# Optimization experiments

Hardware: AMD Instinct MI355X
Metric: run time of the kernel (lower is better)

The kernel has to match this reference:

```python
import jax, jax.numpy as jnp
import numpy as np

SHAPES = ((96, 144), (48, 72), (24, 36), (12, 18))
BS, EMBED = 2, 256
HEADS, LEVELS, POINTS = 8, 4, 4
NEMBED = EMBED // HEADS
LEN_V = sum(h * w for h, w in SHAPES)
LEN_Q = LEN_V  # encoder self-attention: every pixel is a query


def _pos_grid_init():
    # Faithful re-implementation of MultiScaleDeformableAttention.pos_grid_init
    thetas = jnp.arange(HEADS, dtype=jnp.float32) * (2.0 * np.pi / HEADS)
    g = jnp.stack([jnp.cos(thetas), jnp.sin(thetas)], -1)
    g = g / jnp.max(jnp.abs(g), axis=-1, keepdims=True)
    g = jnp.tile(g.reshape(HEADS, 1, 1, 2), (1, LEVELS, POINTS, 1))
    scale = (jnp.arange(POINTS, dtype=jnp.float32) + 1.0)[None, None, :, None]
    return g * scale  # [HEADS, LEVELS, POINTS, 2]


def setup_inputs() -> dict:
    ks = jax.random.split(jax.random.key(0), 7)
    return {
        'query': jax.random.normal(ks[0], (BS, LEN_Q, EMBED), jnp.float32),
        'ref_points': jax.random.uniform(ks[1], (BS, LEN_Q, LEVELS, 2), jnp.float32),
        'value': jax.random.normal(ks[2], (BS, LEN_V, EMBED), jnp.float32),
        'pad_mask': jnp.ones((BS, LEN_V), dtype=bool),
        'value_proj_kernel': jax.random.normal(ks[3], (EMBED, HEADS, NEMBED), jnp.float32) * 0.05,
        'value_proj_bias': jnp.zeros((HEADS, NEMBED), jnp.float32),
        'sampling_offsets_kernel': jax.random.normal(ks[4], (EMBED, HEADS, LEVELS, POINTS, 2), jnp.float32) * 0.01,
        'sampling_offsets_bias': _pos_grid_init(),
        'attn_kernel': jax.random.normal(ks[5], (EMBED, HEADS, LEVELS * POINTS), jnp.float32) * 0.02,
        'attn_bias': jnp.zeros((HEADS, LEVELS * POINTS), jnp.float32),
        'out_kernel': jax.random.normal(ks[6], (HEADS, NEMBED, EMBED), jnp.float32) * 0.05,
        'out_bias': jnp.zeros((EMBED,), jnp.float32),
        'train': 0,
    }


def _bilinear(im, grid, w, h):
    """Batched 2D bilinear interpolation, zero outside the image.

    im:   [B, h*w, e] flattened feature map
    grid: [B, N, 2] normalized coords (pixel centers at (x+0.5)/w, (y+0.5)/h)
    Returns [B, N, e]. Identical math to the original gather-based kernel:
    out-of-bounds corner weights are zeroed, so zero-padding the image by 1
    reproduces the 'empty'-pad + masked-weight scheme exactly.
    """
    B, _, e = im.shape
    imp = jnp.pad(im.reshape(B, h, w, e), ((0, 0), (1, 1), (1, 1), (0, 0)))
    imp = imp.reshape(B, (h + 2) * (w + 2), e)
    x = grid[..., 0] * w - 0.5
    y = grid[..., 1] * h - 0.5
    x0 = jnp.floor(x).astype(jnp.int32)
    y0 = jnp.floor(y).astype(jnp.int32)
    x1 = x0 + 1
    y1 = y0 + 1

    def gather(yy, xx):
        idx = jnp.clip(yy + 1, 0, h + 1) * (w + 2) + jnp.clip(xx + 1, 0, w + 1)
        return jnp.take_along_axis(imp, idx[..., None], axis=1)  # [B, N, e]

    x0f, y0f = x0.astype(x.dtype), y0.astype(y.dtype)
    x1f, y1f = x1.astype(x.dtype), y1.astype(y.dtype)
    inx0 = (x0 >= 0) & (x0 <= w - 1)
    inx1 = (x1 >= 0) & (x1 <= w - 1)
    iny0 = (y0 >= 0) & (y0 <= h - 1)
    iny1 = (y1 >= 0) & (y1 <= h - 1)
    wa = jnp.where(inx0 & iny0, (x1f - x) * (y1f - y), 0.0)
    wb = jnp.where(inx0 & iny1, (x1f - x) * (y - y0f), 0.0)
    wc = jnp.where(inx1 & iny0, (x - x0f) * (y1f - y), 0.0)
    wd = jnp.where(inx1 & iny1, (x - x0f) * (y - y0f), 0.0)
    return (gather(y0, x0) * wa[..., None] + gather(y1, x0) * wb[..., None]
            + gather(y0, x1) * wc[..., None] + gather(y1, x1) * wd[..., None])


def _forward(query, ref_points, value, pad_mask, vpk, vpb, sok, sob, ak, ab, okern, obias):
    bs, len_q, _ = query.shape
    len_v = value.shape[1]
    # value projection + pad masking -> [bs*H, len_v, nembed]
    v = jnp.einsum('bve,ehd->bvhd', value, vpk) + vpb
    v = jnp.where(pad_mask[..., None, None], v, 0)
    v = v.transpose(0, 2, 1, 3).reshape(bs * HEADS, len_v, NEMBED)
    # sampling locations (ref_dim == 2 branch) -> [bs*H, L, P*len_q, 2]
    off = jnp.einsum('bqe,ehlpc->bqhlpc', query, sok) + sob
    offset_norm = jnp.array([[w, h] for h, w in SHAPES], dtype=query.dtype)  # [L, 2]
    loc = ref_points[:, :, None, :, None, :] + off / offset_norm[None, None, None, :, None, :]
    loc = loc.transpose(0, 2, 3, 4, 1, 5).reshape(bs * HEADS, LEVELS, POINTS * len_q, 2)
    # attention weights (softmax over L*P) -> [bs*H, len_q, L*P]
    aw = jnp.einsum('bqe,ehm->bqhm', query, ak) + ab
    aw = jax.nn.softmax(aw, axis=-1)
    aw = aw.transpose(0, 2, 1, 3).reshape(bs * HEADS, len_q, LEVELS * POINTS)
    # per-level bilinear sampling, concatenated level-major over (level, point)
    starts = np.cumsum([0] + [h * w for h, w in SHAPES])
    sampled = []
    for li, (h, w) in enumerate(SHAPES):
        vl = v[:, starts[li]:starts[li + 1], :]
        s = _bilinear(vl, loc[:, li], w, h)  # [bs*H, P*len_q, nembed]
        sampled.append(s.reshape(bs * HEADS, POINTS, len_q, NEMBED))
    sampled = jnp.concatenate(sampled, axis=1)  # [bs*H, L*P, len_q, nembed]
    x = jnp.einsum('blqe,bql->bqe', sampled, aw)
    x = x.reshape(bs, HEADS, len_q, NEMBED)
    # output projection: DenseGeneral over (heads, nembed)
    return jnp.einsum('bhqe,hed->bqd', x, okern) + obias


def reference(query, ref_points, value, pad_mask, value_proj_kernel, value_proj_bias,
              sampling_offsets_kernel, sampling_offsets_bias, attn_kernel, attn_bias,
              out_kernel, out_bias, train):
    del train  # eval mode (no remat); math is identical
    return _forward(query, ref_points, value, pad_mask, value_proj_kernel, value_proj_bias,
                    sampling_offsets_kernel, sampling_offsets_bias, attn_kernel, attn_bias,
                    out_kernel, out_bias)
```

## Files before the change

kernel.cpp:

```cpp
#include <hip/hip_runtime.h>
#include <math.h>

#define LEN 18360
#define M_ROWS (2 * LEN)
#define NTASK (16 * LEN)

typedef unsigned short u16;
typedef __attribute__((ext_vector_type(8))) short bf16x8;
typedef __attribute__((ext_vector_type(4))) float f32x4;

__device__ __forceinline__ u16 f2bf(float f) {
  unsigned u = __float_as_uint(f);
  return (u16)((u + 0x7fffu + ((u >> 16) & 1u)) >> 16);
}
__device__ __forceinline__ u16 f2h(float f) {
  union { _Float16 h; u16 u; } c;
  c.h = (_Float16)f;
  return c.u;
}
__device__ __forceinline__ void async_cp16(const void* g, void* l) {
  __builtin_amdgcn_global_load_lds(
      (const __attribute__((address_space(1))) unsigned*)g,
      (__attribute__((address_space(3))) unsigned*)l, 16, 0, 0);
}

#define MIX_LO(acc, word, wf)                                           \
  asm("v_fma_mix_f32 %0, %1, %2, %0 op_sel:[0,0,0] op_sel_hi:[1,0,0]"  \
      : "+v"(acc)                                                       \
      : "v"(word), "v"(wf))
#define MIX_HI(acc, word, wf)                                           \
  asm("v_fma_mix_f32 %0, %1, %2, %0 op_sel:[1,0,0] op_sel_hi:[1,0,0]"  \
      : "+v"(acc)                                                       \
      : "v"(word), "v"(wf))

__global__ __launch_bounds__(256) void gemm_mfma_k(
    const u16* __restrict__ A0, const u16* __restrict__ Bt0,
    const float* __restrict__ bias0, void* __restrict__ C0, int N0, int nt0,
    int mode0, int split, const u16* __restrict__ A1,
    const u16* __restrict__ Bt1, const float* __restrict__ bias1,
    void* __restrict__ C1, int N1, int nt1, int mode1) {
  __shared__ u16 A_lds[2][8 * 512];
  __shared__ u16 B_lds[2][8 * 512];

  int bid = (int)blockIdx.x;
  const u16* A;
  const u16* Bt;
  const float* bias;
  void* Cv;
  int N, nt, mode;
  if (bid < split) {
    A = A0; Bt = Bt0; bias = bias0; Cv = C0; N = N0; nt = nt0; mode = mode0;
  } else {
    bid -= split;
    A = A1; Bt = Bt1; bias = bias1; Cv = C1; N = N1; nt = nt1; mode = mode1;
  }
  const int n0 = (bid % nt) << 7;
  const int m0 = (bid / nt) << 7;

  const int tid = threadIdx.x;
  const int w = tid >> 6;
  const int lane = tid & 63;
  const int wm = w & 1, wn = w >> 1;
  const int mr = lane & 15;
  const int kq = (lane >> 4) * 8;

  const int st0 = 2 * w;
  const int ga0 = min(m0 + st0 * 16 + mr, M_ROWS - 1);
  const int ga1 = min(m0 + (st0 + 1) * 16 + mr, M_ROWS - 1);
  const int gb0 = n0 + st0 * 16 + mr;
  const int gb1 = n0 + (st0 + 1) * 16 + mr;
  const u16* pa0 = A + (size_t)ga0 * 256 + kq;
  const u16* pa1 = A + (size_t)ga1 * 256 + kq;
  const u16* pb0 = Bt + (size_t)gb0 * 256 + kq;
  const u16* pb1 = Bt + (size_t)gb1 * 256 + kq;

  f32x4 acc[4][4];
#pragma unroll
  for (int i = 0; i < 4; i++)
#pragma unroll
    for (int j = 0; j < 4; j++) acc[i][j] = (f32x4){0.f, 0.f, 0.f, 0.f};

  async_cp16(pa0, &A_lds[0][st0 * 512]);
  async_cp16(pa1, &A_lds[0][(st0 + 1) * 512]);
  async_cp16(pb0, &B_lds[0][st0 * 512]);
  async_cp16(pb1, &B_lds[0][(st0 + 1) * 512]);
  __syncthreads();

#pragma unroll
  for (int kt = 0; kt < 8; kt++) {
    const int cur = kt & 1;
    if (kt < 7) {
      const int k0 = (kt + 1) << 5;
      async_cp16(pa0 + k0, &A_lds[cur ^ 1][st0 * 512]);
      async_cp16(pa1 + k0, &A_lds[cur ^ 1][(st0 + 1) * 512]);
      async_cp16(pb0 + k0, &B_lds[cur ^ 1][st0 * 512]);
      async_cp16(pb1 + k0, &B_lds[cur ^ 1][(st0 + 1) * 512]);
    }
    bf16x8 af[4], bf[4];
#pragma unroll
    for (int i = 0; i < 4; i++)
      af[i] = *(const bf16x8*)&A_lds[cur][(wm * 4 + i) * 512 + lane * 8];
#pragma unroll
    for (int j = 0; j < 4; j++)
      bf[j] = *(const bf16x8*)&B_lds[cur][(wn * 4 + j) * 512 + lane * 8];
#pragma unroll
    for (int i = 0; i < 4; i++)
#pragma unroll
      for (int j = 0; j < 4; j++)
        acc[i][j] = __builtin_amdgcn_mfma_f32_16x16x32_bf16(bf[j], af[i],
                                                            acc[i][j], 0, 0, 0);
    if (kt < 7) __syncthreads();
  }

#pragma unroll
  for (int i = 0; i < 4; i++) {
    const int row = m0 + wm * 64 + i * 16 + mr;
    if (row >= M_ROWS) continue;
#pragma unroll
    for (int j = 0; j < 4; j++) {
      const int col = n0 + wn * 64 + j * 16 + (lane >> 4) * 4;
      const float4 b4 = *(const float4*)(bias + col);
      float4 o;
      o.x = acc[i][j][0] + b4.x;
      o.y = acc[i][j][1] + b4.y;
      o.z = acc[i][j][2] + b4.z;
      o.w = acc[i][j][3] + b4.w;
      if (mode == 0) {
        *(float4*)((float*)Cv + (size_t)row * N + col) = o;
      } else if (mode == 1) {
        const int b = row >= LEN;
        const int lv = row - b * LEN;
        const int h = col >> 5, d = col & 31;
        uint2 p;
        p.x = (unsigned)f2h(o.x) | ((unsigned)f2h(o.y) << 16);
        p.y = (unsigned)f2h(o.z) | ((unsigned)f2h(o.w) << 16);
        *(uint2*)((u16*)Cv + ((size_t)((b * 8 + h) * LEN + lv)) * 32 + d) = p;
      } else {
        uint2 p;
        p.x = (unsigned)f2bf(o.x) | ((unsigned)f2bf(o.y) << 16);
        p.y = (unsigned)f2bf(o.z) | ((unsigned)f2bf(o.w) << 16);
        *(uint2*)((u16*)Cv + (size_t)row * N + col) = p;
      }
    }
  }
}

__global__ __launch_bounds__(256) void cast_qv_k(const float* __restrict__ q,
                                                 const float* __restrict__ v,
                                                 u16* __restrict__ qb,
                                                 u16* __restrict__ vb) {
  const size_t i = ((size_t)blockIdx.x * 256 + threadIdx.x) * 4;
  float4 a = *(const float4*)(q + i);
  uint2 p;
  p.x = (unsigned)f2bf(a.x) | ((unsigned)f2bf(a.y) << 16);
  p.y = (unsigned)f2bf(a.z) | ((unsigned)f2bf(a.w) << 16);
  *(uint2*)&qb[i] = p;
  float4 c = *(const float4*)(v + i);
  p.x = (unsigned)f2bf(c.x) | ((unsigned)f2bf(c.y) << 16);
  p.y = (unsigned)f2bf(c.z) | ((unsigned)f2bf(c.w) << 16);
  *(uint2*)&vb[i] = p;
}

__global__ __launch_bounds__(256) void wcast_k(
    const float* __restrict__ vpk, const float* __restrict__ sok,
    const float* __restrict__ ak, const float* __restrict__ ok,
    const float* __restrict__ sob, const float* __restrict__ ab,
    u16* __restrict__ vpk_t, u16* __restrict__ sa_t, u16* __restrict__ ok_t,
    float* __restrict__ bias_cat) {
  const int gid = blockIdx.x * 256 + threadIdx.x;
  if (gid < 65536) {
    const int d = gid, n = d >> 8, k = d & 255;
    vpk_t[d] = f2bf(vpk[k * 256 + n]);
  } else if (gid < 131072) {
    const int d = gid - 65536, n = d >> 8, k = d & 255;
    sa_t[d] = f2bf(sok[k * 256 + n]);
  } else if (gid < 163840) {
    const int d = gid - 131072, n = d >> 8, k = d & 255;
    sa_t[65536 + d] = f2bf(ak[k * 128 + n]);
  } else if (gid < 229376) {
    const int d = gid - 163840, n = d >> 8, k = d & 255;
    ok_t[d] = f2bf(ok[k * 256 + n]);
  } else if (gid < 229760) {
    const int d = gid - 229376;
    bias_cat[d] = (d < 256) ? sob[d] : ab[d - 256];
  }
}

__global__ __launch_bounds__(256) void sampler_k(
    const u16* __restrict__ v,
    const u16* __restrict__ offaw,
    const float* __restrict__ refp,
    u16* __restrict__ xb)
{
  __shared__ int2 meta[4 * 544];
  const int tid = threadIdx.x;
  const int wv = tid >> 6;
  const int lane = tid & 63;
  int2* const mw = &meta[wv * 544];

  const int bid0 = (int)blockIdx.x;
  const int xcd = bid0 & 7;
  const int within = bid0 >> 3;
  const int bid =
      (xcd < 4 ? xcd * 1148 : 4 * 1148 + (xcd - 4) * 1147) + within;

#pragma unroll
  for (int rep = 0; rep < 2; rep++) {
    const int t4 = lane >> 4;
    const int s = lane & 15;
    const int l = s >> 2;
    const int tl = (rep << 2) + t4;

    const int task = (bid << 5) + (wv << 3) + tl;
    const int q = task % LEN;
// ... 78 lines not shown
      mA2 = mrowA[s + 1];
      mB2 = mrowB[s + 1];
      pA2 = *(const uint4*)(vb + (unsigned)mA2.x + dqo);
      pB2 = *(const uint4*)(vb + (unsigned)mB2.x + dqo);
    }
    const float wA = __int_as_float(mA.y);
    const float wB = __int_as_float(mB.y);
    MIX_LO(a0, pA.x, wA);
    MIX_HI(a1, pA.x, wA);
    MIX_LO(a2, pA.y, wA);
    MIX_HI(a3, pA.y, wA);
    MIX_LO(a4, pA.z, wA);
    MIX_HI(a5, pA.z, wA);
    MIX_LO(a6, pA.w, wA);
    MIX_HI(a7, pA.w, wA);
    MIX_LO(a0, pB.x, wB);
    MIX_HI(a1, pB.x, wB);
    MIX_LO(a2, pB.y, wB);
    MIX_HI(a3, pB.y, wB);
    MIX_LO(a4, pB.z, wB);
    MIX_HI(a5, pB.z, wB);
    MIX_LO(a6, pB.w, wB);
    MIX_HI(a7, pB.w, wB);
    mA = mA2; mB = mB2; pA = pA2; pB = pB2;
  }

  a0 += __shfl_xor(a0, 4); a1 += __shfl_xor(a1, 4);
  a2 += __shfl_xor(a2, 4); a3 += __shfl_xor(a3, 4);
  a4 += __shfl_xor(a4, 4); a5 += __shfl_xor(a5, 4);
  a6 += __shfl_xor(a6, 4); a7 += __shfl_xor(a7, 4);

  if (c2 == 0) {
    uint4 o;
    o.x = (unsigned)f2bf(a0) | ((unsigned)f2bf(a1) << 16);
    o.y = (unsigned)f2bf(a2) | ((unsigned)f2bf(a3) << 16);
    o.z = (unsigned)f2bf(a4) | ((unsigned)f2bf(a5) << 16);
    o.w = (unsigned)f2bf(a6) | ((unsigned)f2bf(a7) << 16);
    *(uint4*)&xb[qrow * 256 + h * 32 + (dq << 3)] = o;
  }
}

extern "C" void kernel_launch(void* const* d_in, const int* in_sizes, int n_in,
                              void* d_out, int out_size, void* d_ws,
                              size_t ws_size, hipStream_t stream) {
  (void)in_sizes; (void)n_in; (void)out_size; (void)ws_size;

  const float* query = (const float*)d_in[0];
  const float* refp = (const float*)d_in[1];
  const float* value = (const float*)d_in[2];
  const float* vpk = (const float*)d_in[4];
  const float* vpb = (const float*)d_in[5];
  const float* sok = (const float*)d_in[6];
  const float* sob = (const float*)d_in[7];
  const float* ak = (const float*)d_in[8];
  const float* ab = (const float*)d_in[9];
  const float* okern = (const float*)d_in[10];
  const float* obias = (const float*)d_in[11];

  char* p = (char*)d_ws;
  u16* v_ws = (u16*)p;   p += (size_t)M_ROWS * 256 * 2;
  u16* offaw = (u16*)p;  p += (size_t)M_ROWS * 384 * 2;
  u16* qbf = (u16*)p;    p += (size_t)M_ROWS * 256 * 2;
  u16* vbf = (u16*)p;    p += (size_t)M_ROWS * 256 * 2;
  u16* vpk_t = (u16*)p;  p += 65536 * 2;
  u16* sa_t = (u16*)p;   p += 98304 * 2;
  u16* ok_t = (u16*)p;   p += 65536 * 2;
  float* bias_cat = (float*)p;
  u16* x_b = qbf;

  const dim3 blk(256);
  const int mt = (M_ROWS + 127) / 128;

  cast_qv_k<<<dim3(2350080 / 256), blk, 0, stream>>>(query, value, qbf, vbf);
  wcast_k<<<dim3(898), blk, 0, stream>>>(vpk, sok, ak, okern, sob, ab, vpk_t,
                                         sa_t, ok_t, bias_cat);
  gemm_mfma_k<<<dim3(2 * mt + 3 * mt), blk, 0, stream>>>(
      vbf, vpk_t, vpb, v_ws, 256, 2, 1, 2 * mt,
      qbf, sa_t, bias_cat, offaw, 384, 3, 2);
  sampler_k<<<dim3(NTASK / 32), blk, 0, stream>>>(v_ws, offaw, refp, x_b);
  gemm_mfma_k<<<dim3(2 * mt), blk, 0, stream>>>(
      x_b, ok_t, obias, (float*)d_out, 256, 2, 0, 2 * mt,
      x_b, ok_t, obias, (float*)d_out, 256, 2, 0);
}
```

Baseline: 254.2 us.

## Fuse fp32-to-bf16 input cast into GEMM A-tile loads and remap blocks per XCD

Removes the separate cast kernel for query and value. The projection GEMM now reads fp32 A rows directly, converts them to bf16 in registers, and writes them to LDS, with the next tile's loads issued before the MFMAs. This saves one launch and a full write and re-read of the bf16 copies. Block IDs are also remapped so that consecutive tiles land on the same XCD, to improve L2 locality. In exchange, the fp32 A loads go through registers instead of async LDS copies, which raises VGPR pressure and adds conversion ALU work inside the GEMM.

Result: no change. 251.7 us (-1.0%).

```diff
diff --git a/kernel.cpp b/kernel.cpp
--- a/kernel.cpp
+++ b/kernel.cpp
@@ -33,26 +33,35 @@
       : "+v"(acc)                                                       \
       : "v"(word), "v"(wf))
 
+__device__ __forceinline__ int xcd_chunk_remap(int bid0, int nwg) {
+  const int q = nwg >> 3, r = nwg & 7;
+  const int xcd = bid0 & 7;
+  const int wi = bid0 >> 3;
+  return (xcd < r ? xcd * (q + 1) : r * (q + 1) + (xcd - r) * q) + wi;
+}
+
 __global__ __launch_bounds__(256) void gemm_mfma_k(
-    const u16* __restrict__ A0, const u16* __restrict__ Bt0,
+    const void* __restrict__ A0, const u16* __restrict__ Bt0,
     const float* __restrict__ bias0, void* __restrict__ C0, int N0, int nt0,
-    int mode0, int split, const u16* __restrict__ A1,
+    int mode0, int af0, int split, const void* __restrict__ A1,
     const u16* __restrict__ Bt1, const float* __restrict__ bias1,
-    void* __restrict__ C1, int N1, int nt1, int mode1) {
+    void* __restrict__ C1, int N1, int nt1, int mode1, int af1) {
   __shared__ u16 A_lds[2][8 * 512];
   __shared__ u16 B_lds[2][8 * 512];
 
-  int bid = (int)blockIdx.x;
-  const u16* A;
+  int bid = xcd_chunk_remap((int)blockIdx.x, (int)gridDim.x);
+  const void* Av;
   const u16* Bt;
   const float* bias;
   void* Cv;
-  int N, nt, mode;
+  int N, nt, mode, af;
   if (bid < split) {
-    A = A0; Bt = Bt0; bias = bias0; Cv = C0; N = N0; nt = nt0; mode = mode0;
+    Av = A0; Bt = Bt0; bias = bias0; Cv = C0; N = N0; nt = nt0; mode = mode0;
+    af = af0;
   } else {
     bid -= split;
-    A = A1; Bt = Bt1; bias = bias1; Cv = C1; N = N1; nt = nt1; mode = mode1;
+    Av = A1; Bt = Bt1; bias = bias1; Cv = C1; N = N1; nt = nt1; mode = mode1;
+    af = af1;
   }
   const int n0 = (bid % nt) << 7;
   const int m0 = (bid / nt) << 7;
@@ -69,10 +78,16 @@
   const int ga1 = min(m0 + (st0 + 1) * 16 + mr, M_ROWS - 1);
   const int gb0 = n0 + st0 * 16 + mr;
   const int gb1 = n0 + (st0 + 1) * 16 + mr;
-  const u16* pa0 = A + (size_t)ga0 * 256 + kq;
-  const u16* pa1 = A + (size_t)ga1 * 256 + kq;
+  const u16* ba0 = (const u16*)Av + (size_t)ga0 * 256 + kq;
+  const u16* ba1 = (const u16*)Av + (size_t)ga1 * 256 + kq;
+  const float* fa0 = (const float*)Av + (size_t)ga0 * 256 + kq;
+  const float* fa1 = (const float*)Av + (size_t)ga1 * 256 + kq;
   const u16* pb0 = Bt + (size_t)gb0 * 256 + kq;
   const u16* pb1 = Bt + (size_t)gb1 * 256 + kq;
+  u16* const la0 = &A_lds[0][st0 * 512 + lane * 8];
+  u16* const la1 = &A_lds[0][(st0 + 1) * 512 + lane * 8];
+  u16* const lb0 = &A_lds[1][st0 * 512 + lane * 8];
+  u16* const lb1 = &A_lds[1][(st0 + 1) * 512 + lane * 8];
 
   f32x4 acc[4][4];
 #pragma unroll
@@ -80,8 +95,26 @@
 #pragma unroll
     for (int j = 0; j < 4; j++) acc[i][j] = (f32x4){0.f, 0.f, 0.f, 0.f};
 
-  async_cp16(pa0, &A_lds[0][st0 * 512]);
-  async_cp16(pa1, &A_lds[0][(st0 + 1) * 512]);
+  if (af) {
+    const float4 f0 = *(const float4*)(fa0);
+    const float4 f1 = *(const float4*)(fa0 + 4);
+    const float4 g0 = *(const float4*)(fa1);
+    const float4 g1 = *(const float4*)(fa1 + 4);
+    uint4 pk;
+    pk.x = (unsigned)f2bf(f0.x) | ((unsigned)f2bf(f0.y) << 16);
+    pk.y = (unsigned)f2bf(f0.z) | ((unsigned)f2bf(f0.w) << 16);
+    pk.z = (unsigned)f2bf(f1.x) | ((unsigned)f2bf(f1.y) << 16);
+    pk.w = (unsigned)f2bf(f1.z) | ((unsigned)f2bf(f1.w) << 16);
+    *(uint4*)la0 = pk;
+    pk.x = (unsigned)f2bf(g0.x) | ((unsigned)f2bf(g0.y) << 16);
+    pk.y = (unsigned)f2bf(g0.z) | ((unsigned)f2bf(g0.w) << 16);
+    pk.z = (unsigned)f2bf(g1.x) | ((unsigned)f2bf(g1.y) << 16);
+    pk.w = (unsigned)f2bf(g1.z) | ((unsigned)f2bf(g1.w) << 16);
+    *(uint4*)la1 = pk;
+  } else {
+    async_cp16(ba0, &A_lds[0][st0 * 512]);
+    async_cp16(ba1, &A_lds[0][(st0 + 1) * 512]);
+  }
   async_cp16(pb0, &B_lds[0][st0 * 512]);
   async_cp16(pb1, &B_lds[0][(st0 + 1) * 512]);
   __syncthreads();
@@ -89,26 +122,47 @@
 #pragma unroll
   for (int kt = 0; kt < 8; kt++) {
     const int cur = kt & 1;
+    const int kn = (kt + 1) << 5;
+    float4 f0, f1, g0, g1;
     if (kt < 7) {
-      const int k0 = (kt + 1) << 5;
-      async_cp16(pa0 + k0, &A_lds[cur ^ 1][st0 * 512]);
-      async_cp16(pa1 + k0, &A_lds[cur ^ 1][(st0 + 1) * 512]);
-      async_cp16(pb0 + k0, &B_lds[cur ^ 1][st0 * 512]);
-      async_cp16(pb1 + k0, &B_lds[cur ^ 1][(st0 + 1) * 512]);
+      if (af) {
+        f0 = *(const float4*)(fa0 + kn);
+        f1 = *(const float4*)(fa0 + kn + 4);
+        g0 = *(const float4*)(fa1 + kn);
+        g1 = *(const float4*)(fa1 + kn + 4);
+      } else {
+        async_cp16(ba0 + kn, &A_lds[cur ^ 1][st0 * 512]);
+        async_cp16(ba1 + kn, &A_lds[cur ^ 1][(st0 + 1) * 512]);
+      }
+      async_cp16(pb0 + kn, &B_lds[cur ^ 1][st0 * 512]);
+      async_cp16(pb1 + kn, &B_lds[cur ^ 1][(st0 + 1) * 512]);
     }
-    bf16x8 af[4], bf[4];
+    bf16x8 afr[4], bfr[4];
 #pragma unroll
     for (int i = 0; i < 4; i++)
-      af[i] = *(const bf16x8*)&A_lds[cur][(wm * 4 + i) * 512 + lane * 8];
+      afr[i] = *(const bf16x8*)&A_lds[cur][(wm * 4 + i) * 512 + lane * 8];
 #pragma unroll
     for (int j = 0; j < 4; j++)
-      bf[j] = *(const bf16x8*)&B_lds[cur][(wn * 4 + j) * 512 + lane * 8];
+      bfr[j] = *(const bf16x8*)&B_lds[cur][(wn * 4 + j) * 512 + lane * 8];
 #pragma unroll
     for (int i = 0; i < 4; i++)
 #pragma unroll
       for (int j = 0; j < 4; j++)
-        acc[i][j] = __builtin_amdgcn_mfma_f32_16x16x32_bf16(bf[j], af[i],
+        acc[i][j] = __builtin_amdgcn_mfma_f32_16x16x32_bf16(bfr[j], afr[i],
                                                             acc[i][j], 0, 0, 0);
+    if (kt < 7 && af) {
+      uint4 pk;
+      pk.x = (unsigned)f2bf(f0.x) | ((unsigned)f2bf(f0.y) << 16);
+      pk.y = (unsigned)f2bf(f0.z) | ((unsigned)f2bf(f0.w) << 16);
+      pk.z = (unsigned)f2bf(f1.x) | ((unsigned)f2bf(f1.y) << 16);
+      pk.w = (unsigned)f2bf(f1.z) | ((unsigned)f2bf(f1.w) << 16);
+      *(uint4*)(cur ? la0 : lb0) = pk;
+      pk.x = (unsigned)f2bf(g0.x) | ((unsigned)f2bf(g0.y) << 16);
+      pk.y = (unsigned)f2bf(g0.z) | ((unsigned)f2bf(g0.w) << 16);
+      pk.z = (unsigned)f2bf(g1.x) | ((unsigned)f2bf(g1.y) << 16);
+      pk.w = (unsigned)f2bf(g1.z) | ((unsigned)f2bf(g1.w) << 16);
+      *(uint4*)(cur ? la1 : lb1) = pk;
+    }
     if (kt < 7) __syncthreads();
   }
 
@@ -143,22 +197,6 @@
       }
     }
   }
-}
-
-__global__ __launch_bounds__(256) void cast_qv_k(const float* __restrict__ q,
-                                                 const float* __restrict__ v,
-                                                 u16* __restrict__ qb,
-                                                 u16* __restrict__ vb) {
-  const size_t i = ((size_t)blockIdx.x * 256 + threadIdx.x) * 4;
-  float4 a = *(const float4*)(q + i);
-  uint2 p;
-  p.x = (unsigned)f2bf(a.x) | ((unsigned)f2bf(a.y) << 16);
-  p.y = (unsigned)f2bf(a.z) | ((unsigned)f2bf(a.w) << 16);
-  *(uint2*)&qb[i] = p;
-  float4 c = *(const float4*)(v + i);
-  p.x = (unsigned)f2bf(c.x) | ((unsigned)f2bf(c.y) << 16);
-  p.y = (unsigned)f2bf(c.z) | ((unsigned)f2bf(c.w) << 16);
-  *(uint2*)&vb[i] = p;
 }
 
 __global__ __launch_bounds__(256) void wcast_k(
@@ -352,25 +390,22 @@
   char* p = (char*)d_ws;
   u16* v_ws = (u16*)p;   p += (size_t)M_ROWS * 256 * 2;
   u16* offaw = (u16*)p;  p += (size_t)M_ROWS * 384 * 2;
-  u16* qbf = (u16*)p;    p += (size_t)M_ROWS * 256 * 2;
-  u16* vbf = (u16*)p;    p += (size_t)M_ROWS * 256 * 2;
+  u16* x_ws = (u16*)p;   p += (size_t)M_ROWS * 256 * 2;
   u16* vpk_t = (u16*)p;  p += 65536 * 2;
   u16* sa_t = (u16*)p;   p += 98304 * 2;
   u16* ok_t = (u16*)p;   p += 65536 * 2;
   float* bias_cat = (float*)p;
-  u16* x_b = qbf;
 
   const dim3 blk(256);
   const int mt = (M_ROWS + 127) / 128;
 
-  cast_qv_k<<<dim3(2350080 / 256), blk, 0, stream>>>(query, value, qbf, vbf);
   wcast_k<<<dim3(898), blk, 0, stream>>>(vpk, sok, ak, okern, sob, ab, vpk_t,
                                          sa_t, ok_t, bias_cat);
   gemm_mfma_k<<<dim3(2 * mt + 3 * mt), blk, 0, stream>>>(
-      vbf, vpk_t, vpb, v_ws, 256, 2, 1, 2 * mt,
-      qbf, sa_t, bias_cat, offaw, 384, 3, 2);
-  sampler_k<<<dim3(NTASK / 32), blk, 0, stream>>>(v_ws, offaw, refp, x_b);
+      value, vpk_t, vpb, v_ws, 256, 2, 1, 1, 2 * mt,
+      query, sa_t, bias_cat, offaw, 384, 3, 2, 1);
+  sampler_k<<<dim3(NTASK / 32), blk, 0, stream>>>(v_ws, offaw, refp, x_ws);
   gemm_mfma_k<<<dim3(2 * mt), blk, 0, stream>>>(
-      x_b, ok_t, obias, (float*)d_out, 256, 2, 0, 2 * mt,
-      x_b, ok_t, obias, (float*)d_out, 256, 2, 0);
-}
+      x_ws, ok_t, obias, (float*)d_out, 256, 2, 0, 0, 2 * mt,
+      x_ws, ok_t, obias, (float*)d_out, 256, 2, 0, 0);
+}
```

## Fuse fp32-to-bf16 cast into persistent GEMM with resident B tiles

Applied to the files above, without the earlier changes.

Removes the separate query/value cast kernel. The first GEMM now loads fp32 activations directly and packs them to bf16 in registers before writing LDS. Both GEMMs become persistent kernels that keep the full 128-column B slice in LDS, loop over several M tiles with register double-buffered A loads, and remap block IDs so that chunks stay on one XCD. This trades a larger LDS footprint (about 80KB per block, lowering occupancy) and fp32 A traffic inside the GEMM for dropping one launch, the bf16 intermediate writes and reads, and repeated B loads.

After: 284.7 us. 12.0% more time.

```diff
diff --git a/kernel.cpp b/kernel.cpp
--- a/kernel.cpp
+++ b/kernel.cpp
@@ -4,14 +4,15 @@
 #define LEN 18360
 #define M_ROWS (2 * LEN)
 #define NTASK (16 * LEN)
+#define MT_TOT 287
 
 typedef unsigned short u16;
 typedef __attribute__((ext_vector_type(8))) short bf16x8;
 typedef __attribute__((ext_vector_type(4))) float f32x4;
 
-__device__ __forceinline__ u16 f2bf(float f) {
+__device__ __forceinline__ unsigned f2bf(float f) {
   unsigned u = __float_as_uint(f);
-  return (u16)((u + 0x7fffu + ((u >> 16) & 1u)) >> 16);
+  return (u + 0x7fffu + ((u >> 16) & 1u)) >> 16;
 }
 __device__ __forceinline__ u16 f2h(float f) {
   union { _Float16 h; u16 u; } c;
@@ -33,29 +34,42 @@
       : "+v"(acc)                                                       \
       : "v"(word), "v"(wf))
 
-__global__ __launch_bounds__(256) void gemm_mfma_k(
-    const u16* __restrict__ A0, const u16* __restrict__ Bt0,
-    const float* __restrict__ bias0, void* __restrict__ C0, int N0, int nt0,
-    int mode0, int split, const u16* __restrict__ A1,
-    const u16* __restrict__ Bt1, const float* __restrict__ bias1,
-    void* __restrict__ C1, int N1, int nt1, int mode1) {
-  __shared__ u16 A_lds[2][8 * 512];
-  __shared__ u16 B_lds[2][8 * 512];
-
-  int bid = (int)blockIdx.x;
-  const u16* A;
+__device__ __forceinline__ int xcd_chunk_remap(int bid0, int nwg) {
+  const int q = nwg >> 3, r = nwg & 7;
+  const int xcd = bid0 & 7;
+  const int wi = bid0 >> 3;
+  return (xcd < r ? xcd * (q + 1) : r * (q + 1) + (xcd - r) * q) + wi;
+}
+
+template <int AF>
+__global__ __launch_bounds__(256) void gemm_persist_k(
+    const void* __restrict__ A0, const u16* __restrict__ Bt0,
+    const float* __restrict__ bias0, void* __restrict__ C0, int N0, int mode0,
+    int lanes0, const void* __restrict__ A1, const u16* __restrict__ Bt1,
+    const float* __restrict__ bias1, void* __restrict__ C1, int N1, int mode1,
+    int NL, int J) {
+  __shared__ u16 B_all[8 * 4096];
+  __shared__ u16 A_lds[2][4096];
+
+  const int r = xcd_chunk_remap((int)blockIdx.x, (int)gridDim.x);
+  const int j = r / NL;
+  const int lane_n = r % NL;
+
+  const void* Av;
   const u16* Bt;
   const float* bias;
   void* Cv;
-  int N, nt, mode;
-  if (bid < split) {
-    A = A0; Bt = Bt0; bias = bias0; Cv = C0; N = N0; nt = nt0; mode = mode0;
+  int N, mode, ncol;
+  if (lane_n < lanes0) {
+    Av = A0; Bt = Bt0; bias = bias0; Cv = C0; N = N0; mode = mode0;
+    ncol = lane_n;
   } else {
-    bid -= split;
-    A = A1; Bt = Bt1; bias = bias1; Cv = C1; N = N1; nt = nt1; mode = mode1;
-  }
-  const int n0 = (bid % nt) << 7;
-  const int m0 = (bid / nt) << 7;
+    Av = A1; Bt = Bt1; bias = bias1; Cv = C1; N = N1; mode = mode1;
+    ncol = lane_n - lanes0;
+  }
+  const int n0 = ncol << 7;
+  const int nmt = (MT_TOT - j + J - 1) / J;
+  const int total = nmt << 3;
 
   const int tid = threadIdx.x;
   const int w = tid >> 6;
@@ -63,102 +77,143 @@
   const int wm = w & 1, wn = w >> 1;
   const int mr = lane & 15;
   const int kq = (lane >> 4) * 8;
-
   const int st0 = 2 * w;
-  const int ga0 = min(m0 + st0 * 16 + mr, M_ROWS - 1);
-  const int ga1 = min(m0 + (st0 + 1) * 16 + mr, M_ROWS - 1);
-  const int gb0 = n0 + st0 * 16 + mr;
-  const int gb1 = n0 + (st0 + 1) * 16 + mr;
-  const u16* pa0 = A + (size_t)ga0 * 256 + kq;
-  const u16* pa1 = A + (size_t)ga1 * 256 + kq;
-  const u16* pb0 = Bt + (size_t)gb0 * 256 + kq;
-  const u16* pb1 = Bt + (size_t)gb1 * 256 + kq;
+
+#pragma unroll
+  for (int kt = 0; kt < 8; kt++) {
+#pragma unroll
+    for (int t = 0; t < 2; t++) {
+      const int st = st0 + t;
+      const int gb = n0 + st * 16 + mr;
+      async_cp16(Bt + (size_t)gb * 256 + kt * 32 + kq,
+                 &B_all[kt * 4096 + st * 512]);
+    }
+  }
+
+  float4 Ef0, Ef1, Eg0, Eg1, Of0, Of1, Og0, Og1;
+  uint4 Ea, Eb, Oa, Ob;
+
+#define LOAD_STEP(u, q0, q1, q2, q3, b0, b1)                          \
+  {                                                                   \
+    const int m0c = (j + ((u) >> 3) * J) << 7;                        \
+    const int ga0c = min(m0c + st0 * 16 + mr, M_ROWS - 1);            \
+    const int ga1c = min(m0c + (st0 + 1) * 16 + mr, M_ROWS - 1);      \
+    const int ko = ((u) & 7) * 32 + kq;                               \
+    if (AF) {                                                         \
+      const float* fA0 = (const float*)Av + (size_t)ga0c * 256 + ko;  \
+      const float* fA1 = (const float*)Av + (size_t)ga1c * 256 + ko;  \
+      q0 = *(const float4*)fA0;                                       \
+      q1 = *(const float4*)(fA0 + 4);                                 \
+      q2 = *(const float4*)fA1;                                       \
+      q3 = *(const float4*)(fA1 + 4);                                 \
+    } else {                                                          \
+      const u16* uA0 = (const u16*)Av + (size_t)ga0c * 256 + ko;      \
+      const u16* uA1 = (const u16*)Av + (size_t)ga1c * 256 + ko;      \
+      b0 = *(const uint4*)uA0;                                        \
+      b1 = *(const uint4*)uA1;                                        \
+    }                                                                 \
+  }
+
+#define PACK_STEP(v, q0, q1, q2, q3, b0, b1)                          \
+  {                                                                   \
+    u16* d0 = &A_lds[(v) & 1][st0 * 512 + lane * 8];                  \
+    u16* d1 = &A_lds[(v) & 1][(st0 + 1) * 512 + lane * 8];            \
+    if (AF) {                                                         \
+      uint4 pk;                                                       \
+      pk.x = f2bf(q0.x) | (f2bf(q0.y) << 16);                         \
+      pk.y = f2bf(q0.z) | (f2bf(q0.w) << 16);                         \
+      pk.z = f2bf(q1.x) | (f2bf(q1.y) << 16);                         \
+      pk.w = f2bf(q1.z) | (f2bf(q1.w) << 16);                         \
+      *(uint4*)d0 = pk;                                               \
+      pk.x = f2bf(q2.x) | (f2bf(q2.y) << 16);                         \
+      pk.y = f2bf(q2.z) | (f2bf(q2.w) << 16);                         \
+      pk.z = f2bf(q3.x) | (f2bf(q3.y) << 16);                         \
+      pk.w = f2bf(q3.z) | (f2bf(q3.w) << 16);                         \
+      *(uint4*)d1 = pk;                                               \
+    } else {                                                          \
+      *(uint4*)d0 = b0;                                               \
+      *(uint4*)d1 = b1;                                               \
+    }                                                                 \
+  }
 
   f32x4 acc[4][4];
 #pragma unroll
   for (int i = 0; i < 4; i++)
 #pragma unroll
-    for (int j = 0; j < 4; j++) acc[i][j] = (f32x4){0.f, 0.f, 0.f, 0.f};
-
-  async_cp16(pa0, &A_lds[0][st0 * 512]);
-  async_cp16(pa1, &A_lds[0][(st0 + 1) * 512]);
-  async_cp16(pb0, &B_lds[0][st0 * 512]);
-  async_cp16(pb1, &B_lds[0][(st0 + 1) * 512]);
+    for (int jj = 0; jj < 4; jj++) acc[i][jj] = (f32x4){0.f, 0.f, 0.f, 0.f};
+
+#define MFMA_STEP(sv)                                                 \
+  {                                                                   \
+    const int kb = ((sv) & 7) * 4096;                                 \
+    bf16x8 afr[4], bfr[4];                                            \
+    _Pragma("unroll") for (int i = 0; i < 4; i++) afr[i] =            \
+        *(const bf16x8*)&A_lds[(sv) & 1][(wm * 4 + i) * 512 + lane * 8]; \
+    _Pragma("unroll") for (int jj = 0; jj < 4; jj++) bfr[jj] =        \
+        *(const bf16x8*)&B_all[kb + (wn * 4 + jj) * 512 + lane * 8];  \
+    _Pragma("unroll") for (int i = 0; i < 4; i++)                     \
+        _Pragma("unroll") for (int jj = 0; jj < 4; jj++) acc[i][jj] = \
+            __builtin_amdgcn_mfma_f32_16x16x32_bf16(bfr[jj], afr[i],  \
+                                                    acc[i][jj], 0, 0, 0); \
+  }
+
+#define EPILOGUE(mtt)                                                 \
+  {                                                                   \
+    const int m0e = (j + (mtt)*J) << 7;                               \
+    _Pragma("unroll") for (int i = 0; i < 4; i++) {                   \
+      const int row = m0e + wm * 64 + i * 16 + mr;                    \
+      if (row < M_ROWS) {                                             \
+        _Pragma("unroll") for (int jj = 0; jj < 4; jj++) {            \
+          const int col = n0 + wn * 64 + jj * 16 + (lane >> 4) * 4;   \
+          const float4 b4 = *(const float4*)(bias + col);             \
+          float4 o;                                                   \
+          o.x = acc[i][jj][0] + b4.x;                                 \
+          o.y = acc[i][jj][1] + b4.y;                                 \
+          o.z = acc[i][jj][2] + b4.z;                                 \
+          o.w = acc[i][jj][3] + b4.w;                                 \
+          if (mode == 0) {                                            \
+            *(float4*)((float*)Cv + (size_t)row * N + col) = o;       \
+          } else if (mode == 1) {                                     \
+            const int bb = row >= LEN;                                \
+            const int lv = row - bb * LEN;                            \
+            const int hh = col >> 5, dd = col & 31;                   \
+            uint2 p;                                                  \
+            p.x = (unsigned)f2h(o.x) | ((unsigned)f2h(o.y) << 16);    \
+            p.y = (unsigned)f2h(o.z) | ((unsigned)f2h(o.w) << 16);    \
+            *(uint2*)((u16*)Cv +                                      \
+                      ((size_t)((bb * 8 + hh) * LEN + lv)) * 32 + dd) = p; \
+          } else {                                                    \
+            uint2 p;                                                  \
+            p.x = f2bf(o.x) | (f2bf(o.y) << 16);                      \
+            p.y = f2bf(o.z) | (f2bf(o.w) << 16);                      \
+            *(uint2*)((u16*)Cv + (size_t)row * N + col) = p;          \
+          }                                                           \
+        }                                                             \
+      }                                                               \
+      _Pragma("unroll") for (int jj = 0; jj < 4; jj++) acc[i][jj] =   \
+          (f32x4){0.f, 0.f, 0.f, 0.f};                                \
+    }                                                                 \
+  }
+
+  LOAD_STEP(0, Ef0, Ef1, Eg0, Eg1, Ea, Eb);
+  LOAD_STEP(1, Of0, Of1, Og0, Og1, Oa, Ob);
+  PACK_STEP(0, Ef0, Ef1, Eg0, Eg1, Ea, Eb);
   __syncthreads();
 
-#pragma unroll
-  for (int kt = 0; kt < 8; kt++) {
-    const int cur = kt & 1;
-    if (kt < 7) {
-      const int k0 = (kt + 1) << 5;
-      async_cp16(pa0 + k0, &A_lds[cur ^ 1][st0 * 512]);
-      async_cp16(pa1 + k0, &A_lds[cur ^ 1][(st0 + 1) * 512]);
-      async_cp16(pb0 + k0, &B_lds[cur ^ 1][st0 * 512]);
-      async_cp16(pb1 + k0, &B_lds[cur ^ 1][(st0 + 1) * 512]);
-    }
-    bf16x8 af[4], bf[4];
-#pragma unroll
-    for (int i = 0; i < 4; i++)
-      af[i] = *(const bf16x8*)&A_lds[cur][(wm * 4 + i) * 512 + lane * 8];
-#pragma unroll
-    for (int j = 0; j < 4; j++)
-      bf[j] = *(const bf16x8*)&B_lds[cur][(wn * 4 + j) * 512 + lane * 8];
-#pragma unroll
-    for (int i = 0; i < 4; i++)
-#pragma unroll
-      for (int j = 0; j < 4; j++)
-        acc[i][j] = __builtin_amdgcn_mfma_f32_16x16x32_bf16(bf[j], af[i],
-                                                            acc[i][j], 0, 0, 0);
-    if (kt < 7) __syncthreads();
-  }
-
-#pragma unroll
-  for (int i = 0; i < 4; i++) {
-    const int row = m0 + wm * 64 + i * 16 + mr;
-    if (row >= M_ROWS) continue;
-#pragma unroll
-    for (int j = 0; j < 4; j++) {
-      const int col = n0 + wn * 64 + j * 16 + (lane >> 4) * 4;
-      const float4 b4 = *(const float4*)(bias + col);
-      float4 o;
-      o.x = acc[i][j][0] + b4.x;
-      o.y = acc[i][j][1] + b4.y;
-      o.z = acc[i][j][2] + b4.z;
-      o.w = acc[i][j][3] + b4.w;
-      if (mode == 0) {
-        *(float4*)((float*)Cv + (size_t)row * N + col) = o;
-      } else if (mode == 1) {
-        const int b = row >= LEN;
-        const int lv = row - b * LEN;
-        const int h = col >> 5, d = col & 31;
-        uint2 p;
-        p.x = (unsigned)f2h(o.x) | ((unsigned)f2h(o.y) << 16);
-        p.y = (unsigned)f2h(o.z) | ((unsigned)f2h(o.w) << 16);
-        *(uint2*)((u16*)Cv + ((size_t)((b * 8 + h) * LEN + lv)) * 32 + d) = p;
-      } else {
-        uint2 p;
-        p.x = (unsigned)f2bf(o.x) | ((unsigned)f2bf(o.y) << 16);
-        p.y = (unsigned)f2bf(o.z) | ((unsigned)f2bf(o.w) << 16);
-        *(uint2*)((u16*)Cv + (size_t)row * N + col) = p;
-      }
-    }
-  }
-}
-
-__global__ __launch_bounds__(256) void cast_qv_k(const float* __restrict__ q,
-                                                 const float* __restrict__ v,
-                                                 u16* __restrict__ qb,
-                                                 u16* __restrict__ vb) {
-  const size_t i = ((size_t)blockIdx.x * 256 + threadIdx.x) * 4;
-  float4 a = *(const float4*)(q + i);
-  uint2 p;
-  p.x = (unsigned)f2bf(a.x) | ((unsigned)f2bf(a.y) << 16);
-  p.y = (unsigned)f2bf(a.z) | ((unsigned)f2bf(a.w) << 16);
-  *(uint2*)&qb[i] = p;
-  float4 c = *(const float4*)(v + i);
-  p.x = (unsigned)f2bf(c.x) | ((unsigned)f2bf(c.y) << 16);
-  p.y = (unsigned)f2bf(c.z) | ((unsigned)f2bf(c.w) << 16);
-  *(uint2*)&vb[i] = p;
+  for (int s = 0; s < total; s += 2) {
+    if (s + 2 < total) LOAD_STEP(s + 2, Ef0, Ef1, Eg0, Eg1, Ea, Eb);
+    MFMA_STEP(s);
+    PACK_STEP(s + 1, Of0, Of1, Og0, Og1, Oa, Ob);
+    __syncthreads();
+    if (s + 3 < total) LOAD_STEP(s + 3, Of0, Of1, Og0, Og1, Oa, Ob);
+    MFMA_STEP(s + 1);
+    if (s + 2 < total) PACK_STEP(s + 2, Ef0, Ef1, Eg0, Eg1, Ea, Eb);
+    if (((s + 1) & 7) == 7) EPILOGUE((s + 1) >> 3);
+    if (s + 2 < total) __syncthreads();
+  }
+#undef LOAD_STEP
+#undef PACK_STEP
+#undef MFMA_STEP
+#undef EPILOGUE
 }
 
 __global__ __launch_bounds__(256) void wcast_k(
@@ -170,16 +225,16 @@
   const int gid = blockIdx.x * 256 + threadIdx.x;
   if (gid < 65536) {
     const int d = gid, n = d >> 8, k = d & 255;
-    vpk_t[d] = f2bf(vpk[k * 256 + n]);
+    vpk_t[d] = (u16)f2bf(vpk[k * 256 + n]);
   } else if (gid < 131072) {
     const int d = gid - 65536, n = d >> 8, k = d & 255;
-    sa_t[d] = f2bf(sok[k * 256 + n]);
+    sa_t[d] = (u16)f2bf(sok[k * 256 + n]);
   } else if (gid < 163840) {
     const int d = gid - 131072, n = d >> 8, k = d & 255;
-    sa_t[65536 + d] = f2bf(ak[k * 128 + n]);
+    sa_t[65536 + d] = (u16)f2bf(ak[k * 128 + n]);
   } else if (gid < 229376) {
     const int d = gid - 163840, n = d >> 8, k = d & 255;
-    ok_t[d] = f2bf(ok[k * 256 + n]);
+    ok_t[d] = (u16)f2bf(ok[k * 256 + n]);
   } else if (gid < 229760) {
     const int d = gid - 229376;
     bias_cat[d] = (d < 256) ? sob[d] : ab[d - 256];
@@ -324,10 +379,10 @@
 
   if (c2 == 0) {
     uint4 o;
-    o.x = (unsigned)f2bf(a0) | ((unsigned)f2bf(a1) << 16);
-    o.y = (unsigned)f2bf(a2) | ((unsigned)f2bf(a3) << 16);
-    o.z = (unsigned)f2bf(a4) | ((unsigned)f2bf(a5) << 16);
-    o.w = (unsigned)f2bf(a6) | ((unsigned)f2bf(a7) << 16);
+    o.x = f2bf(a0) | (f2bf(a1) << 16);
+    o.y = f2bf(a2) | (f2bf(a3) << 16);
+    o.z = f2bf(a4) | (f2bf(a5) << 16);
+    o.w = f2bf(a6) | (f2bf(a7) << 16);
     *(uint4*)&xb[qrow * 256 + h * 32 + (dq << 3)] = o;
   }
 }
@@ -352,25 +407,21 @@
   char* p = (char*)d_ws;
   u16* v_ws = (u16*)p;   p += (size_t)M_ROWS * 256 * 2;
   u16* offaw = (u16*)p;  p += (size_t)M_ROWS * 384 * 2;
-  u16* qbf = (u16*)p;    p += (size_t)M_ROWS * 256 * 2;
-  u16* vbf = (u16*)p;    p += (size_t)M_ROWS * 256 * 2;
+  u16* x_ws = (u16*)p;   p += (size_t)M_ROWS * 256 * 2;
   u16* vpk_t = (u16*)p;  p += 65536 * 2;
   u16* sa_t = (u16*)p;   p += 98304 * 2;
   u16* ok_t = (u16*)p;   p += 65536 * 2;
   float* bias_cat = (float*)p;
-  u16* x_b = qbf;
 
   const dim3 blk(256);
-  const int mt = (M_ROWS + 127) / 128;
-
-  cast_qv_k<<<dim3(2350080 / 256), blk, 0, stream>>>(query, value, qbf, vbf);
+
   wcast_k<<<dim3(898), blk, 0, stream>>>(vpk, sok, ak, okern, sob, ab, vpk_t,
                                          sa_t, ok_t, bias_cat);
-  gemm_mfma_k<<<dim3(2 * mt + 3 * mt), blk, 0, stream>>>(
-      vbf, vpk_t, vpb, v_ws, 256, 2, 1, 2 * mt,
-      qbf, sa_t, bias_cat, offaw, 384, 3, 2);
-  sampler_k<<<dim3(NTASK / 32), blk, 0, stream>>>(v_ws, offaw, refp, x_b);
-  gemm_mfma_k<<<dim3(2 * mt), blk, 0, stream>>>(
-      x_b, ok_t, obias, (float*)d_out, 256, 2, 0, 2 * mt,
-      x_b, ok_t, obias, (float*)d_out, 256, 2, 0);
-}
+  gemm_persist_k<1><<<dim3(510), blk, 0, stream>>>(
+      value, vpk_t, vpb, v_ws, 256, 1, 2,
+      query, sa_t, bias_cat, offaw, 384, 2, 5, 102);
+  sampler_k<<<dim3(NTASK / 32), blk, 0, stream>>>(v_ws, offaw, refp, x_ws);
+  gemm_persist_k<0><<<dim3(512), blk, 0, stream>>>(
+      x_ws, ok_t, obias, (float*)d_out, 256, 0, 2,
+      x_ws, ok_t, obias, (float*)d_out, 256, 0, 2, 256);
+}
```

## Fuse fp32-to-bf16 input cast into GEMM, preload full K in LDS, remap blocks per XCD

Applied to the files above, without the earlier changes.

Removes the separate query/value cast kernel. The projection GEMM now reads fp32 activations directly and converts them to bf16 while storing into LDS, which avoids writing and re-reading the bf16 copies in global memory. The GEMM loads the whole K=256 strip for A and B into LDS up front instead of double-buffering, so the per-step barriers go away, but LDS per block rises to 128 KB and occupancy drops. Block IDs are remapped so that each XCD works on a contiguous chunk of row tiles, with the column tiles of one row tile kept together, to improve L2 reuse.

Result: slower. 283.7 us (+11.6%).

```diff
diff --git a/kernel.cpp b/kernel.cpp
--- a/kernel.cpp
+++ b/kernel.cpp
@@ -4,14 +4,15 @@
 #define LEN 18360
 #define M_ROWS (2 * LEN)
 #define NTASK (16 * LEN)
+#define MT_TOT 287
 
 typedef unsigned short u16;
 typedef __attribute__((ext_vector_type(8))) short bf16x8;
 typedef __attribute__((ext_vector_type(4))) float f32x4;
 
-__device__ __forceinline__ u16 f2bf(float f) {
+__device__ __forceinline__ unsigned f2bf(float f) {
   unsigned u = __float_as_uint(f);
-  return (u16)((u + 0x7fffu + ((u >> 16) & 1u)) >> 16);
+  return (u + 0x7fffu + ((u >> 16) & 1u)) >> 16;
 }
 __device__ __forceinline__ u16 f2h(float f) {
   union { _Float16 h; u16 u; } c;
@@ -22,6 +23,14 @@
   __builtin_amdgcn_global_load_lds(
       (const __attribute__((address_space(1))) unsigned*)g,
       (__attribute__((address_space(3))) unsigned*)l, 16, 0, 0);
+}
+__device__ __forceinline__ uint4 pack8(float4 a, float4 b) {
+  uint4 pk;
+  pk.x = f2bf(a.x) | (f2bf(a.y) << 16);
+  pk.y = f2bf(a.z) | (f2bf(a.w) << 16);
+  pk.z = f2bf(b.x) | (f2bf(b.y) << 16);
+  pk.w = f2bf(b.z) | (f2bf(b.w) << 16);
+  return pk;
 }
 
 #define MIX_LO(acc, word, wf)                                           \
@@ -33,29 +42,41 @@
       : "+v"(acc)                                                       \
       : "v"(word), "v"(wf))
 
-__global__ __launch_bounds__(256) void gemm_mfma_k(
-    const u16* __restrict__ A0, const u16* __restrict__ Bt0,
-    const float* __restrict__ bias0, void* __restrict__ C0, int N0, int nt0,
-    int mode0, int split, const u16* __restrict__ A1,
-    const u16* __restrict__ Bt1, const float* __restrict__ bias1,
-    void* __restrict__ C1, int N1, int nt1, int mode1) {
-  __shared__ u16 A_lds[2][8 * 512];
-  __shared__ u16 B_lds[2][8 * 512];
-
-  int bid = (int)blockIdx.x;
-  const u16* A;
+__device__ __forceinline__ int xcd_chunk_remap(int bid0, int nwg) {
+  const int q = nwg >> 3, r = nwg & 7;
+  const int xcd = bid0 & 7;
+  const int wi = bid0 >> 3;
+  return (xcd < r ? xcd * (q + 1) : r * (q + 1) + (xcd - r) * q) + wi;
+}
+
+template <int AF>
+__global__ __launch_bounds__(256) void gemm_full_k(
+    const void* __restrict__ A0, const u16* __restrict__ Bt0,
+    const float* __restrict__ bias0, void* __restrict__ C0, int N0, int mode0,
+    int lanes0, const void* __restrict__ A1, const u16* __restrict__ Bt1,
+    const float* __restrict__ bias1, void* __restrict__ C1, int N1, int mode1,
+    int NL) {
+  __shared__ u16 B_all[8 * 4096];
+  __shared__ u16 A_all[8 * 4096];
+
+  const int r = xcd_chunk_remap((int)blockIdx.x, (int)gridDim.x);
+  const int j = r / NL;
+  const int lane_n = r % NL;
+
+  const void* Av;
   const u16* Bt;
   const float* bias;
   void* Cv;
-  int N, nt, mode;
-  if (bid < split) {
-    A = A0; Bt = Bt0; bias = bias0; Cv = C0; N = N0; nt = nt0; mode = mode0;
+  int N, mode, ncol;
+  if (lane_n < lanes0) {
+    Av = A0; Bt = Bt0; bias = bias0; Cv = C0; N = N0; mode = mode0;
+    ncol = lane_n;
   } else {
-    bid -= split;
-    A = A1; Bt = Bt1; bias = bias1; Cv = C1; N = N1; nt = nt1; mode = mode1;
-  }
-  const int n0 = (bid % nt) << 7;
-  const int m0 = (bid / nt) << 7;
+    Av = A1; Bt = Bt1; bias = bias1; Cv = C1; N = N1; mode = mode1;
+    ncol = lane_n - lanes0;
+  }
+  const int n0 = ncol << 7;
+  const int m0 = j << 7;
 
   const int tid = threadIdx.x;
   const int w = tid >> 6;
@@ -63,53 +84,71 @@
   const int wm = w & 1, wn = w >> 1;
   const int mr = lane & 15;
   const int kq = (lane >> 4) * 8;
-
   const int st0 = 2 * w;
+
   const int ga0 = min(m0 + st0 * 16 + mr, M_ROWS - 1);
   const int ga1 = min(m0 + (st0 + 1) * 16 + mr, M_ROWS - 1);
   const int gb0 = n0 + st0 * 16 + mr;
   const int gb1 = n0 + (st0 + 1) * 16 + mr;
-  const u16* pa0 = A + (size_t)ga0 * 256 + kq;
-  const u16* pa1 = A + (size_t)ga1 * 256 + kq;
-  const u16* pb0 = Bt + (size_t)gb0 * 256 + kq;
-  const u16* pb1 = Bt + (size_t)gb1 * 256 + kq;
+
+#pragma unroll
+  for (int kt = 0; kt < 8; kt++) {
+    async_cp16(Bt + (size_t)gb0 * 256 + kt * 32 + kq,
+               &B_all[kt * 4096 + st0 * 512]);
+    async_cp16(Bt + (size_t)gb1 * 256 + kt * 32 + kq,
+               &B_all[kt * 4096 + (st0 + 1) * 512]);
+    if (!AF) {
+      async_cp16((const u16*)Av + (size_t)ga0 * 256 + kt * 32 + kq,
+                 &A_all[kt * 4096 + st0 * 512]);
+      async_cp16((const u16*)Av + (size_t)ga1 * 256 + kt * 32 + kq,
+                 &A_all[kt * 4096 + (st0 + 1) * 512]);
+    }
+  }
+  if (AF) {
+    const float* fa0 = (const float*)Av + (size_t)ga0 * 256 + kq;
+    const float* fa1 = (const float*)Av + (size_t)ga1 * 256 + kq;
+#pragma unroll
+    for (int kp = 0; kp < 8; kp += 2) {
+      const float4 e0 = *(const float4*)(fa0 + kp * 32);
+      const float4 e1 = *(const float4*)(fa0 + kp * 32 + 4);
+      const float4 e2 = *(const float4*)(fa1 + kp * 32);
+      const float4 e3 = *(const float4*)(fa1 + kp * 32 + 4);
+      const float4 o0 = *(const float4*)(fa0 + kp * 32 + 32);
+      const float4 o1 = *(const float4*)(fa0 + kp * 32 + 36);
+      const float4 o2 = *(const float4*)(fa1 + kp * 32 + 32);
+      const float4 o3 = *(const float4*)(fa1 + kp * 32 + 36);
+      *(uint4*)&A_all[kp * 4096 + st0 * 512 + lane * 8] = pack8(e0, e1);
+      *(uint4*)&A_all[kp * 4096 + (st0 + 1) * 512 + lane * 8] = pack8(e2, e3);
+      *(uint4*)&A_all[(kp + 1) * 4096 + st0 * 512 + lane * 8] = pack8(o0, o1);
+      *(uint4*)&A_all[(kp + 1) * 4096 + (st0 + 1) * 512 + lane * 8] =
+          pack8(o2, o3);
+    }
+  }
 
   f32x4 acc[4][4];
 #pragma unroll
   for (int i = 0; i < 4; i++)
 #pragma unroll
-    for (int j = 0; j < 4; j++) acc[i][j] = (f32x4){0.f, 0.f, 0.f, 0.f};
-
-  async_cp16(pa0, &A_lds[0][st0 * 512]);
-  async_cp16(pa1, &A_lds[0][(st0 + 1) * 512]);
-  async_cp16(pb0, &B_lds[0][st0 * 512]);
-  async_cp16(pb1, &B_lds[0][(st0 + 1) * 512]);
+    for (int jj = 0; jj < 4; jj++) acc[i][jj] = (f32x4){0.f, 0.f, 0.f, 0.f};
+
   __syncthreads();
 
 #pragma unroll
   for (int kt = 0; kt < 8; kt++) {
-    const int cur = kt & 1;
-    if (kt < 7) {
-      const int k0 = (kt + 1) << 5;
-      async_cp16(pa0 + k0, &A_lds[cur ^ 1][st0 * 512]);
-      async_cp16(pa1 + k0, &A_lds[cur ^ 1][(st0 + 1) * 512]);
-      async_cp16(pb0 + k0, &B_lds[cur ^ 1][st0 * 512]);
-      async_cp16(pb1 + k0, &B_lds[cur ^ 1][(st0 + 1) * 512]);
-    }
-    bf16x8 af[4], bf[4];
+    bf16x8 afr[4], bfr[4];
 #pragma unroll
     for (int i = 0; i < 4; i++)
-      af[i] = *(const bf16x8*)&A_lds[cur][(wm * 4 + i) * 512 + lane * 8];
-#pragma unroll
-    for (int j = 0; j < 4; j++)
-      bf[j] = *(const bf16x8*)&B_lds[cur][(wn * 4 + j) * 512 + lane * 8];
+      afr[i] = *(const bf16x8*)&A_all[kt * 4096 + (wm * 4 + i) * 512 + lane * 8];
+#pragma unroll
+    for (int jj = 0; jj < 4; jj++)
+      bfr[jj] =
+          *(const bf16x8*)&B_all[kt * 4096 + (wn * 4 + jj) * 512 + lane * 8];
 #pragma unroll
     for (int i = 0; i < 4; i++)
 #pragma unroll
-      for (int j = 0; j < 4; j++)
-        acc[i][j] = __builtin_amdgcn_mfma_f32_16x16x32_bf16(bf[j], af[i],
-                                                            acc[i][j], 0, 0, 0);
-    if (kt < 7) __syncthreads();
+      for (int jj = 0; jj < 4; jj++)
+        acc[i][jj] = __builtin_amdgcn_mfma_f32_16x16x32_bf16(bfr[jj], afr[i],
+                                                             acc[i][jj], 0, 0, 0);
   }
 
 #pragma unroll
@@ -117,48 +156,32 @@
     const int row = m0 + wm * 64 + i * 16 + mr;
     if (row >= M_ROWS) continue;
 #pragma unroll
-    for (int j = 0; j < 4; j++) {
-      const int col = n0 + wn * 64 + j * 16 + (lane >> 4) * 4;
+    for (int jj = 0; jj < 4; jj++) {
+      const int col = n0 + wn * 64 + jj * 16 + (lane >> 4) * 4;
       const float4 b4 = *(const float4*)(bias + col);
       float4 o;
-      o.x = acc[i][j][0] + b4.x;
-      o.y = acc[i][j][1] + b4.y;
-      o.z = acc[i][j][2] + b4.z;
-      o.w = acc[i][j][3] + b4.w;
+      o.x = acc[i][jj][0] + b4.x;
+      o.y = acc[i][jj][1] + b4.y;
+      o.z = acc[i][jj][2] + b4.z;
+      o.w = acc[i][jj][3] + b4.w;
       if (mode == 0) {
         *(float4*)((float*)Cv + (size_t)row * N + col) = o;
       } else if (mode == 1) {
-        const int b = row >= LEN;
-        const int lv = row - b * LEN;
-        const int h = col >> 5, d = col & 31;
+        const int bb = row >= LEN;
+        const int lv = row - bb * LEN;
+        const int hh = col >> 5, dd = col & 31;
         uint2 p;
         p.x = (unsigned)f2h(o.x) | ((unsigned)f2h(o.y) << 16);
         p.y = (unsigned)f2h(o.z) | ((unsigned)f2h(o.w) << 16);
-        *(uint2*)((u16*)Cv + ((size_t)((b * 8 + h) * LEN + lv)) * 32 + d) = p;
+        *(uint2*)((u16*)Cv + ((size_t)((bb * 8 + hh) * LEN + lv)) * 32 + dd) = p;
       } else {
         uint2 p;
-        p.x = (unsigned)f2bf(o.x) | ((unsigned)f2bf(o.y) << 16);
-        p.y = (unsigned)f2bf(o.z) | ((unsigned)f2bf(o.w) << 16);
+        p.x = f2bf(o.x) | (f2bf(o.y) << 16);
+        p.y = f2bf(o.z) | (f2bf(o.w) << 16);
         *(uint2*)((u16*)Cv + (size_t)row * N + col) = p;
       }
     }
   }
-}
-
-__global__ __launch_bounds__(256) void cast_qv_k(const float* __restrict__ q,
-                                                 const float* __restrict__ v,
-                                                 u16* __restrict__ qb,
-                                                 u16* __restrict__ vb) {
-  const size_t i = ((size_t)blockIdx.x * 256 + threadIdx.x) * 4;
-  float4 a = *(const float4*)(q + i);
-  uint2 p;
-  p.x = (unsigned)f2bf(a.x) | ((unsigned)f2bf(a.y) << 16);
-  p.y = (unsigned)f2bf(a.z) | ((unsigned)f2bf(a.w) << 16);
-  *(uint2*)&qb[i] = p;
-  float4 c = *(const float4*)(v + i);
-  p.x = (unsigned)f2bf(c.x) | ((unsigned)f2bf(c.y) << 16);
-  p.y = (unsigned)f2bf(c.z) | ((unsigned)f2bf(c.w) << 16);
-  *(uint2*)&vb[i] = p;
 }
 
 __global__ __launch_bounds__(256) void wcast_k(
@@ -170,16 +193,16 @@
   const int gid = blockIdx.x * 256 + threadIdx.x;
   if (gid < 65536) {
     const int d = gid, n = d >> 8, k = d & 255;
-    vpk_t[d] = f2bf(vpk[k * 256 + n]);
+    vpk_t[d] = (u16)f2bf(vpk[k * 256 + n]);
   } else if (gid < 131072) {
     const int d = gid - 65536, n = d >> 8, k = d & 255;
-    sa_t[d] = f2bf(sok[k * 256 + n]);
+    sa_t[d] = (u16)f2bf(sok[k * 256 + n]);
   } else if (gid < 163840) {
     const int d = gid - 131072, n = d >> 8, k = d & 255;
-    sa_t[65536 + d] = f2bf(ak[k * 128 + n]);
+    sa_t[65536 + d] = (u16)f2bf(ak[k * 128 + n]);
   } else if (gid < 229376) {
     const int d = gid - 163840, n = d >> 8, k = d & 255;
-    ok_t[d] = f2bf(ok[k * 256 + n]);
+    ok_t[d] = (u16)f2bf(ok[k * 256 + n]);
   } else if (gid < 229760) {
     const int d = gid - 229376;
     bias_cat[d] = (d < 256) ? sob[d] : ab[d - 256];
@@ -324,10 +347,10 @@
 
   if (c2 == 0) {
     uint4 o;
-    o.x = (unsigned)f2bf(a0) | ((unsigned)f2bf(a1) << 16);
-    o.y = (unsigned)f2bf(a2) | ((unsigned)f2bf(a3) << 16);
-    o.z = (unsigned)f2bf(a4) | ((unsigned)f2bf(a5) << 16);
-    o.w = (unsigned)f2bf(a6) | ((unsigned)f2bf(a7) << 16);
+    o.x = f2bf(a0) | (f2bf(a1) << 16);
+    o.y = f2bf(a2) | (f2bf(a3) << 16);
+    o.z = f2bf(a4) | (f2bf(a5) << 16);
+    o.w = f2bf(a6) | (f2bf(a7) << 16);
     *(uint4*)&xb[qrow * 256 + h * 32 + (dq << 3)] = o;
   }
 }
@@ -352,25 +375,21 @@
   char* p = (char*)d_ws;
   u16* v_ws = (u16*)p;   p += (size_t)M_ROWS * 256 * 2;
   u16* offaw = (u16*)p;  p += (size_t)M_ROWS * 384 * 2;
-  u16* qbf = (u16*)p;    p += (size_t)M_ROWS * 256 * 2;
-  u16* vbf = (u16*)p;    p += (size_t)M_ROWS * 256 * 2;
+  u16* x_ws = (u16*)p;   p += (size_t)M_ROWS * 256 * 2;
   u16* vpk_t = (u16*)p;  p += 65536 * 2;
   u16* sa_t = (u16*)p;   p += 98304 * 2;
   u16* ok_t = (u16*)p;   p += 65536 * 2;
   float* bias_cat = (float*)p;
-  u16* x_b = qbf;
 
   const dim3 blk(256);
-  const int mt = (M_ROWS + 127) / 128;
-
-  cast_qv_k<<<dim3(2350080 / 256), blk, 0, stream>>>(query, value, qbf, vbf);
+
   wcast_k<<<dim3(898), blk, 0, stream>>>(vpk, sok, ak, okern, sob, ab, vpk_t,
                                          sa_t, ok_t, bias_cat);
-  gemm_mfma_k<<<dim3(2 * mt + 3 * mt), blk, 0, stream>>>(
-      vbf, vpk_t, vpb, v_ws, 256, 2, 1, 2 * mt,
-      qbf, sa_t, bias_cat, offaw, 384, 3, 2);
-  sampler_k<<<dim3(NTASK / 32), blk, 0, stream>>>(v_ws, offaw, refp, x_b);
-  gemm_mfma_k<<<dim3(2 * mt), blk, 0, stream>>>(
-      x_b, ok_t, obias, (float*)d_out, 256, 2, 0, 2 * mt,
-      x_b, ok_t, obias, (float*)d_out, 256, 2, 0);
-}
+  gemm_full_k<1><<<dim3(MT_TOT * 5), blk, 0, stream>>>(
+      value, vpk_t, vpb, v_ws, 256, 1, 2,
+      query, sa_t, bias_cat, offaw, 384, 2, 5);
+  sampler_k<<<dim3(NTASK / 32), blk, 0, stream>>>(v_ws, offaw, refp, x_ws);
+  gemm_full_k<0><<<dim3(MT_TOT * 2), blk, 0, stream>>>(
+      x_ws, ok_t, obias, (float*)d_out, 256, 0, 2,
+      x_ws, ok_t, obias, (float*)d_out, 256, 0, 2);
+}
```
